# Optimization experiments

Hardware: AMD Instinct MI355X
Metric: run time of the kernel (lower is better)

Reference implementation:

```python
import jax, jax.numpy as jnp
import numpy as np

T, B, D_POSE, H, K_CODES = 30, 1024, 135, 512, 512
EPS = 1e-5


def _bn_relu(x, g, b):
    # BatchNorm1d (training-mode batch stats, biased var) + ReLU; x: (B, C, L)
    m = x.mean(axis=(0, 2), keepdims=True)
    v = x.var(axis=(0, 2), keepdims=True)
    y = g[None, :, None] * (x - m) * jax.lax.rsqrt(v + EPS) + b[None, :, None]
    return jax.nn.relu(y)


def _conv_sk(x, w):
    # Conv1d with stride == kernel_size (non-overlapping): pure reshaped GEMM.
    # x: (B, I, L), w: (O, I, K) torch layout -> (B, O, L//K)
    Bn, I, L = x.shape
    O, _, K = w.shape
    xr = x.reshape(Bn, I, L // K, K)
    return jnp.einsum('bitk,oik->bot', xr, w)


def _convT_sk(x, w):
    # ConvTranspose1d with stride == kernel_size: x (B, I, L), w (I, O, K) torch layout
    Bn, I, L = x.shape
    _, O, K = w.shape
    return jnp.einsum('bil,iok->bolk', x, w).reshape(Bn, O, L * K)


def setup_inputs() -> dict:
    key = jax.random.key(0)
    ks = jax.random.split(key, 12)
    sc = 0.05
    inp = {
        'input_seqs': jax.random.normal(ks[0], (T, B, D_POSE), jnp.float32),
        'W_in': jax.random.normal(ks[1], (D_POSE, H), jnp.float32) * sc,
        'b_in': jnp.zeros((H,), jnp.float32),
        'w_e1': jax.random.normal(ks[2], (H, H, 5), jnp.float32) * sc,
        'g_e1': jnp.ones((H,), jnp.float32), 'b_e1': jnp.zeros((H,), jnp.float32),
        'w_e2': jax.random.normal(ks[3], (H, H, 3), jnp.float32) * sc,
        'g_e2': jnp.ones((H,), jnp.float32), 'b_e2': jnp.zeros((H,), jnp.float32),
        'w_e3': jax.random.normal(ks[4], (H, H, 2), jnp.float32) * sc,
        'g_e3': jnp.ones((H,), jnp.float32), 'b_e3': jnp.zeros((H,), jnp.float32),
        'codebook': jax.random.normal(ks[5], (K_CODES, H), jnp.float32) * sc,
        'W_q': jax.random.normal(ks[6], (H, H), jnp.float32) * sc,
        'b_q': jnp.zeros((H,), jnp.float32),
        'w_d1': jax.random.normal(ks[7], (H, H, 2), jnp.float32) * sc,
        'g_d1': jnp.ones((H,), jnp.float32), 'b_d1': jnp.zeros((H,), jnp.float32),
        'w_d2': jax.random.normal(ks[8], (H, H, 3), jnp.float32) * sc,
        'g_d2': jnp.ones((H,), jnp.float32), 'b_d2': jnp.zeros((H,), jnp.float32),
        'w_d3': jax.random.normal(ks[9], (H, H, 5), jnp.float32) * sc,
        'g_d3': jnp.ones((H,), jnp.float32), 'b_d3': jnp.zeros((H,), jnp.float32),
        'W_out': jax.random.normal(ks[10], (H, D_POSE), jnp.float32) * sc,
        'b_out': jnp.zeros((D_POSE,), jnp.float32),
    }
    return inp


def reference(input_seqs, W_in, b_in, w_e1, g_e1, b_e1, w_e2, g_e2, b_e2,
              w_e3, g_e3, b_e3, codebook, W_q, b_q,
              w_d1, g_d1, b_d1, w_d2, g_d2, b_d2, w_d3, g_d3, b_d3,
              W_out, b_out):
    commitment_cost = 0.25
    # ---- EncoderCNN ----
    h = input_seqs @ W_in + b_in              # (T, B, H)
    h = jnp.transpose(h, (1, 2, 0))           # (B, H, T)
    h = _bn_relu(_conv_sk(h, w_e1), g_e1, b_e1)   # (B, H, 6)
    h = _bn_relu(_conv_sk(h, w_e2), g_e2, b_e2)   # (B, H, 2)
    z = _bn_relu(_conv_sk(h, w_e3), g_e3, b_e3)   # (B, H, 1)

    # ---- VQ (VQ_Payam, straight-through) ----
    Bn, D, L = z.shape
    flat = jnp.transpose(z, (0, 2, 1)).reshape(-1, D)            # (B*L, D)
    dist = (jnp.sum(flat ** 2, axis=1, keepdims=True)
            + jnp.sum(codebook ** 2, axis=1)
            - 2.0 * flat @ codebook.T)                           # (B*L, K)
    idx = jnp.argmin(dist, axis=1)                               # (B*L,)
    quantized = codebook[idx]                                    # (B*L, D)
    e_latent_loss = jnp.mean((jax.lax.stop_gradient(quantized) - flat) ** 2)
    q_latent_loss = jnp.mean((quantized - jax.lax.stop_gradient(flat)) ** 2)
    vq_loss = q_latent_loss + commitment_cost * e_latent_loss
    q_st = flat + jax.lax.stop_gradient(quantized - flat)        # straight-through
    avg_probs = jnp.mean(jax.nn.one_hot(idx, K_CODES, dtype=flat.dtype), axis=0)
    perplexity = jnp.exp(-jnp.sum(avg_probs * jnp.log(avg_probs + 1e-10)))

    # ---- DecoderCNN ----
    d = q_st @ W_q + b_q                      # (B, H)
    d = d[:, :, None]                         # (B, H, 1)
    d = _bn_relu(_convT_sk(d, w_d1), g_d1, b_d1)  # (B, H, 2)
    d = _bn_relu(_convT_sk(d, w_d2), g_d2, b_d2)  # (B, H, 6)
    d = _bn_relu(_convT_sk(d, w_d3), g_d3, b_d3)  # (B, H, 30)
    recon = jnp.transpose(d, (0, 2, 1)) @ W_out + b_out           # (B, T, D_POSE)
    return recon, vq_loss, perplexity
```

## Files before the change

### kernel.cpp

```cpp
#include <hip/hip_runtime.h>
#include <math.h>


#define TM 64
#define TN 64
#define BK 32
#define LSTR 68

typedef __attribute__((ext_vector_type(8))) short bf16x8;
typedef __attribute__((ext_vector_type(4))) float f32x4;

__device__ __forceinline__ unsigned pk_bf16(float a, float b) {
    unsigned ua = __float_as_uint(a), ub = __float_as_uint(b);
    ua += 0x7fffu + ((ua >> 16) & 1u);
    ub += 0x7fffu + ((ub >> 16) & 1u);
    return (ua >> 16) | (ub & 0xffff0000u);
}
__device__ __forceinline__ unsigned short bfh(float x) {
    unsigned u = __float_as_uint(x);
    u += 0x7fffu + ((u >> 16) & 1u);
    return (unsigned short)(u >> 16);
}
__device__ __forceinline__ float bf2f(unsigned short h) {
    return __uint_as_float(((unsigned)h) << 16);
}

template <int NV>
__device__ __forceinline__ void bn_on_raw(uint4* raw, int kbase,
                                          const float* __restrict__ bnS,
                                          const float* __restrict__ bnB) {
#pragma unroll
    for (int i = 0; i < NV; ++i) {
        unsigned* u4 = (unsigned*)&raw[i];
#pragma unroll
        for (int j = 0; j < 4; ++j) {
            const int k = kbase + (i << 3) + (j << 1);
            unsigned u = u4[j];
            float x0 = __uint_as_float(u << 16);
            float x1 = __uint_as_float(u & 0xffff0000u);
            x0 = fmaxf(fmaf(x0, bnS[k],     bnB[k]),     0.f);
            x1 = fmaxf(fmaf(x1, bnS[k + 1], bnB[k + 1]), 0.f);
            u4[j] = pk_bf16(x0, x1);
        }
    }
}

__global__ __launch_bounds__(256)
void k_gemm(const float* __restrict__ Abase,
            const float* __restrict__ Wt,
            float* __restrict__ Cout,
            const float* __restrict__ bias,
            const float* __restrict__ bnS, const float* __restrict__ bnB,
            float* __restrict__ stats,
            unsigned long long* __restrict__ amin,
            const float* __restrict__ codesq,
            int Mslice, int K, int N,
            int n_terms, int enc_mode, int decK)
{
    __shared__ __align__(16) float As[BK][LSTR];
    __shared__ __align__(16) float Bs[BK][LSTR];
    __shared__ float colsum[TN];
    __shared__ float colsq[TN];

    const int tid = threadIdx.x;
    const int z  = blockIdx.z;
    const int n0 = blockIdx.x * TN;
    const int m0 = blockIdx.y * TM;
    const int ty = tid >> 4;
    const int tx = tid & 15;

    if (stats != nullptr && tid < TN) { colsum[tid] = 0.f; colsq[tid] = 0.f; }

    float acc[4][4];
#pragma unroll
    for (int i = 0; i < 4; ++i)
#pragma unroll
        for (int j = 0; j < 4; ++j) acc[i][j] = 0.f;

    const int arow = tid >> 2;
    const int ac4  = (tid & 3) << 2;
    const int brow = tid >> 3;
    const int bc4  = (tid & 7) << 2;

    int mrow = m0 + arow;
    if (mrow > Mslice - 1) mrow = Mslice - 1;

    const bool alignedK = ((K & 31) == 0);

    for (int term = 0; term < n_terms; ++term) {
        int a_slice, wk;
        if (enc_mode) { a_slice = z * n_terms + term; wk = term; }
        else          { a_slice = z / decK;           wk = z % decK; }
        const float* Ap = Abase + (size_t)a_slice * (size_t)Mslice * (size_t)K;
        const float* Wp = Wt    + (size_t)wk * (size_t)K * (size_t)N;
        const float* Arow_p = Ap + (size_t)mrow * (size_t)K;

        for (int k0 = 0; k0 < K; k0 += BK) {
            __syncthreads();
            if (alignedK) {
                float4 a0 = *(const float4*)(Arow_p + k0 + ac4);
                float4 a1 = *(const float4*)(Arow_p + k0 + ac4 + 16);
                if (bnS != nullptr) {
                    float4 s0 = *(const float4*)(bnS + k0 + ac4);
                    float4 c0 = *(const float4*)(bnB + k0 + ac4);
                    float4 s1 = *(const float4*)(bnS + k0 + ac4 + 16);
                    float4 c1 = *(const float4*)(bnB + k0 + ac4 + 16);
                    a0.x = fmaxf(fmaf(a0.x, s0.x, c0.x), 0.f);
                    a0.y = fmaxf(fmaf(a0.y, s0.y, c0.y), 0.f);
                    a0.z = fmaxf(fmaf(a0.z, s0.z, c0.z), 0.f);
                    a0.w = fmaxf(fmaf(a0.w, s0.w, c0.w), 0.f);
                    a1.x = fmaxf(fmaf(a1.x, s1.x, c1.x), 0.f);
                    a1.y = fmaxf(fmaf(a1.y, s1.y, c1.y), 0.f);
                    a1.z = fmaxf(fmaf(a1.z, s1.z, c1.z), 0.f);
                    a1.w = fmaxf(fmaf(a1.w, s1.w, c1.w), 0.f);
                }
                As[ac4+0][arow] = a0.x;  As[ac4+1][arow] = a0.y;
                As[ac4+2][arow] = a0.z;  As[ac4+3][arow] = a0.w;
                As[ac4+16][arow] = a1.x; As[ac4+17][arow] = a1.y;
                As[ac4+18][arow] = a1.z; As[ac4+19][arow] = a1.w;
            } else {
#pragma unroll
                for (int j = 0; j < 4; ++j) {
                    int k = k0 + ac4 + j;
                    As[ac4+j][arow] = (k < K) ? Arow_p[k] : 0.f;
                    int k2 = k + 16;
                    As[ac4+16+j][arow] = (k2 < K) ? Arow_p[k2] : 0.f;
                }
            }
            {
                int kB = k0 + brow;
                float4 b0 = make_float4(0.f, 0.f, 0.f, 0.f);
                float4 b1 = make_float4(0.f, 0.f, 0.f, 0.f);
                if (kB < K) {
                    const float* wrow = Wp + (size_t)kB * N + n0;
                    b0 = *(const float4*)(wrow + bc4);
                    b1 = *(const float4*)(wrow + bc4 + 32);
                }
                *(float4*)&Bs[brow][bc4]      = b0;
                *(float4*)&Bs[brow][bc4 + 32] = b1;
            }
            __syncthreads();
#pragma unroll
            for (int kk = 0; kk < BK; ++kk) {
                float4 av = *(const float4*)&As[kk][ty << 2];
                float4 bv = *(const float4*)&Bs[kk][tx << 2];
                acc[0][0] = fmaf(av.x, bv.x, acc[0][0]);
                acc[0][1] = fmaf(av.x, bv.y, acc[0][1]);
                acc[0][2] = fmaf(av.x, bv.z, acc[0][2]);
                acc[0][3] = fmaf(av.x, bv.w, acc[0][3]);
                acc[1][0] = fmaf(av.y, bv.x, acc[1][0]);
                acc[1][1] = fmaf(av.y, bv.y, acc[1][1]);
                acc[1][2] = fmaf(av.y, bv.z, acc[1][2]);
                acc[1][3] = fmaf(av.y, bv.w, acc[1][3]);
                acc[2][0] = fmaf(av.z, bv.x, acc[2][0]);
                acc[2][1] = fmaf(av.z, bv.y, acc[2][1]);
                acc[2][2] = fmaf(av.z, bv.z, acc[2][2]);
                acc[2][3] = fmaf(av.z, bv.w, acc[2][3]);
                acc[3][0] = fmaf(av.w, bv.x, acc[3][0]);
                acc[3][1] = fmaf(av.w, bv.y, acc[3][1]);
                acc[3][2] = fmaf(av.w, bv.z, acc[3][2]);
                acc[3][3] = fmaf(av.w, bv.w, acc[3][3]);
            }
        }
    }

    if (amin != nullptr) {
        float4 cq = *(const float4*)(codesq + n0 + (tx << 2));
#pragma unroll
        for (int i = 0; i < 4; ++i) {
            int m = m0 + (ty << 2) + i;
            if (m >= Mslice) continue;
            float d0 = cq.x - 2.f * acc[i][0];
            float d1 = cq.y - 2.f * acc[i][1];
            float d2 = cq.z - 2.f * acc[i][2];
            float d3 = cq.w - 2.f * acc[i][3];
            float best = d0; int bj = 0;
            if (d1 < best) { best = d1; bj = 1; }
            if (d2 < best) { best = d2; bj = 2; }
            if (d3 < best) { best = d3; bj = 3; }
            unsigned u = __float_as_uint(best);
            u = (u & 0x80000000u) ? ~u : (u | 0x80000000u);
            unsigned long long key =
                ((unsigned long long)u << 32) | (unsigned)(n0 + (tx << 2) + bj);
            atomicMin(&amin[m], key);
        }
        return;
    }

#pragma unroll
    for (int i = 0; i < 4; ++i) {
        int m = m0 + (ty << 2) + i;
        if (m >= Mslice) continue;
        float4 v = make_float4(acc[i][0], acc[i][1], acc[i][2], acc[i][3]);
        if (bias != nullptr) {
            float4 bb = *(const float4*)(bias + n0 + (tx << 2));
            v.x += bb.x; v.y += bb.y; v.z += bb.z; v.w += bb.w;
        }
        *(float4*)&Cout[((size_t)z * Mslice + m) * N + n0 + (tx << 2)] = v;
    }

    if (stats != nullptr) {
#pragma unroll
        for (int j = 0; j < 4; ++j) {
            float s = 0.f, q = 0.f;
#pragma unroll
            for (int i = 0; i < 4; ++i) {
                int m = m0 + (ty << 2) + i;
                if (m < Mslice) { float x = acc[i][j]; s += x; q += x * x; }
            }
            atomicAdd(&colsum[(tx << 2) + j], s);
            atomicAdd(&colsq [(tx << 2) + j], q);
        }
        __syncthreads();
        if (tid < TN) {
            atomicAdd(&stats[n0 + tid],       colsum[tid]);
            atomicAdd(&stats[512 + n0 + tid], colsq[tid]);
        }
    }
}

#define ASTR 72

__global__ __launch_bounds__(256)
void k_mfma_b(const unsigned short* __restrict__ Abase,
              const unsigned short* __restrict__ Bt,
              unsigned short* __restrict__ Cb,
              float* __restrict__ operm,
              const float* __restrict__ bias,
              const float* __restrict__ bnS, const float* __restrict__ bnB,
              float* __restrict__ stats,
              int Mslice, int K, int N, int decK)
{
    __shared__ __align__(16) unsigned short As[128 * ASTR];
    __shared__ __align__(16) unsigned short Bs[128 * ASTR];
    __shared__ float colsum[128], colsq[128];

    const int tid  = threadIdx.x;
    const int lane = tid & 63;
    const int wave = tid >> 6;
    const int wm = (wave >> 1) << 6;
    const int wn = (wave & 1) << 6;
    const int z  = blockIdx.z;
    const int n0 = blockIdx.x << 7;
    const int m0 = blockIdx.y << 7;

    if (stats != nullptr && tid < 128) { colsum[tid] = 0.f; colsq[tid] = 0.f; }

    const int a_slice = z / decK, wk = z - a_slice * decK;
    const unsigned short* Ap = Abase + (size_t)a_slice * (size_t)Mslice * (size_t)K;
    const unsigned short* Bp = Bt + (size_t)wk * (size_t)N * (size_t)K;

    const int sr = tid >> 1;
    const int sk = (tid & 1) << 5;

    const unsigned short* Arow = Ap + (size_t)(m0 + sr) * K + sk;
    const unsigned short* Brow = Bp + (size_t)(n0 + sr) * K + sk;
    const bool bvalid = (n0 + sr) < N;

    f32x4 acc[4][4];
#pragma unroll
    for (int i = 0; i < 4; ++i)
#pragma unroll
        for (int j = 0; j < 4; ++j) acc[i][j] = (f32x4){0.f, 0.f, 0.f, 0.f};

    const int lidx = lane & 15;
    const int lq   = lane >> 4;

    uint4 pa[4], pb[4];
#pragma unroll
    for (int i = 0; i < 4; ++i) pa[i] = *(const uint4*)(Arow + (i << 3));
    if (bnS != nullptr) bn_on_raw<4>(pa, sk, bnS, bnB);
    if (bvalid) {
#pragma unroll
        for (int i = 0; i < 4; ++i) pb[i] = *(const uint4*)(Brow + (i << 3));
    } else {
#pragma unroll
        for (int i = 0; i < 4; ++i) pb[i] = make_uint4(0u, 0u, 0u, 0u);
    }

    for (int k0 = 0; k0 < K; k0 += 64) {
        __syncthreads();
        {
            uint4* dA = (uint4*)&As[sr * ASTR + sk];
            uint4* dB = (uint4*)&Bs[sr * ASTR + sk];
#pragma unroll
            for (int i = 0; i < 4; ++i) { dA[i] = pa[i]; dB[i] = pb[i]; }
        }
        const int k0n = k0 + 64;
        if (k0n < K) {
#pragma unroll
            for (int i = 0; i < 4; ++i) pa[i] = *(const uint4*)(Arow + k0n + (i << 3));
            if (bnS != nullptr) bn_on_raw<4>(pa, k0n + sk, bnS, bnB);
            if (bvalid) {
#pragma unroll
                for (int i = 0; i < 4; ++i) pb[i] = *(const uint4*)(Brow + k0n + (i << 3));
            }
        }
        __syncthreads();
#pragma unroll
        for (int ks = 0; ks < 2; ++ks) {
            const int kb = (ks << 5) + (lq << 3);
            bf16x8 af[4], bfv[4];
#pragma unroll
            for (int t = 0; t < 4; ++t)
                af[t] = *(const bf16x8*)&As[(wm + (t << 4) + lidx) * ASTR + kb];
#pragma unroll
            for (int t = 0; t < 4; ++t)
                bfv[t] = *(const bf16x8*)&Bs[(wn + (t << 4) + lidx) * ASTR + kb];
#pragma unroll
            for (int mt = 0; mt < 4; ++mt)
#pragma unroll
                for (int nt = 0; nt < 4; ++nt)
                    acc[mt][nt] = __builtin_amdgcn_mfma_f32_16x16x32_bf16(
                        af[mt], bfv[nt], acc[mt][nt], 0, 0, 0);
        }
    }

    const int rbase = lq << 2;
#pragma unroll
    for (int nt = 0; nt < 4; ++nt) {
        const int col = n0 + wn + (nt << 4) + lidx;
        const float badd = (bias != nullptr && col < N) ? bias[col] : 0.f;
        float s = 0.f, q = 0.f;
#pragma unroll
        for (int mt = 0; mt < 4; ++mt) {
#pragma unroll
            for (int r = 0; r < 4; ++r) {
                float x = acc[mt][nt][r];
                s += x; q += x * x;
                const int row = m0 + wm + (mt << 4) + rbase + r;
                if (operm != nullptr) {
                    if (col < N) {
                        const int t = row >> 10, b = row & 1023;
                        operm[(size_t)b * 4050 + t * 135 + col] = x + badd;
                    }
                } else {
                    Cb[((size_t)z * Mslice + row) * (size_t)N + col] = bfh(x + badd);
                }
            }
        }
        if (stats != nullptr) {
            s += __shfl_xor(s, 16, 64); s += __shfl_xor(s, 32, 64);
            q += __shfl_xor(q, 16, 64); q += __shfl_xor(q, 32, 64);
            if (lq == 0) {
                atomicAdd(&colsum[wn + (nt << 4) + lidx], s);
                atomicAdd(&colsq [wn + (nt << 4) + lidx], q);
            }
        }
    }
    if (stats != nullptr) {
        __syncthreads();
        if (tid < 128) {
            atomicAdd(&stats[n0 + tid],       colsum[tid]);
            atomicAdd(&stats[512 + n0 + tid], colsq[tid]);
        }
    }
}

#define BSTR 72

__global__ __launch_bounds__(256)
void k_b64(const unsigned short* __restrict__ Abase,
           const unsigned short* __restrict__ Bt,
           unsigned short* __restrict__ Cb,
           const float* __restrict__ bias,
           const float* __restrict__ bnS, const float* __restrict__ bnB,
           float* __restrict__ stats,
           int Mslice, int K, int N, int decK)
{
    __shared__ __align__(16) unsigned short As[64 * BSTR];
    __shared__ __align__(16) unsigned short Bs[64 * BSTR];
    __shared__ float colsum[64], colsq[64];

    const int tid  = threadIdx.x;
    const int lane = tid & 63;
    const int wave = tid >> 6;
    const int wm = (wave >> 1) << 5;
    const int wn = (wave & 1) << 5;
    const int z  = blockIdx.z;
    const int n0 = blockIdx.x << 6;
    const int m0 = blockIdx.y << 6;

    if (stats != nullptr && tid < 64) { colsum[tid] = 0.f; colsq[tid] = 0.f; }

    const int a_slice = z / decK, wk = z - a_slice * decK;
    const unsigned short* Ap = Abase + (size_t)a_slice * (size_t)Mslice * (size_t)K;
    const unsigned short* Bp = Bt + (size_t)wk * (size_t)N * (size_t)K;

    const int sr = tid >> 2;
    const int sk = (tid & 3) << 4;

    const unsigned short* Arow = Ap + (size_t)(m0 + sr) * K + sk;
    const unsigned short* Brow = Bp + (size_t)(n0 + sr) * K + sk;

    f32x4 acc[2][2];
#pragma unroll
    for (int i = 0; i < 2; ++i)
#pragma unroll
        for (int j = 0; j < 2; ++j) acc[i][j] = (f32x4){0.f, 0.f, 0.f, 0.f};

    const int lidx = lane & 15;
    const int lq   = lane >> 4;

    uint4 pa[2], pb[2];
    pa[0] = *(const uint4*)(Arow);
    pa[1] = *(const uint4*)(Arow + 8);
    if (bnS != nullptr) bn_on_raw<2>(pa, sk, bnS, bnB);
    pb[0] = *(const uint4*)(Brow);
    pb[1] = *(const uint4*)(Brow + 8);

    for (int k0 = 0; k0 < K; k0 += 64) {
        __syncthreads();
        {
            uint4* dA = (uint4*)&As[sr * BSTR + sk];
            uint4* dB = (uint4*)&Bs[sr * BSTR + sk];
            dA[0] = pa[0]; dA[1] = pa[1];
            dB[0] = pb[0]; dB[1] = pb[1];
        }
        const int k0n = k0 + 64;
        if (k0n < K) {
            pa[0] = *(const uint4*)(Arow + k0n);
            pa[1] = *(const uint4*)(Arow + k0n + 8);
            if (bnS != nullptr) bn_on_raw<2>(pa, k0n + sk, bnS, bnB);
            pb[0] = *(const uint4*)(Brow + k0n);
            pb[1] = *(const uint4*)(Brow + k0n + 8);
        }
        __syncthreads();
#pragma unroll
        for (int ks = 0; ks < 2; ++ks) {
            const int kb = (ks << 5) + (lq << 3);
            bf16x8 af[2], bfv[2];
#pragma unroll
            for (int t = 0; t < 2; ++t)
                af[t] = *(const bf16x8*)&As[(wm + (t << 4) + lidx) * BSTR + kb];
#pragma unroll
            for (int t = 0; t < 2; ++t)
                bfv[t] = *(const bf16x8*)&Bs[(wn + (t << 4) + lidx) * BSTR + kb];
#pragma unroll
            for (int mt = 0; mt < 2; ++mt)
#pragma unroll
                for (int nt = 0; nt < 2; ++nt)
                    acc[mt][nt] = __builtin_amdgcn_mfma_f32_16x16x32_bf16(
                        af[mt], bfv[nt], acc[mt][nt], 0, 0, 0);
        }
    }

    const int rbase = lq << 2;
#pragma unroll
    for (int nt = 0; nt < 2; ++nt) {
        const int col = n0 + wn + (nt << 4) + lidx;
        const float badd = (bias != nullptr) ? bias[col] : 0.f;
        float s = 0.f, q = 0.f;
#pragma unroll
        for (int mt = 0; mt < 2; ++mt) {
#pragma unroll
            for (int r = 0; r < 4; ++r) {
                float x = acc[mt][nt][r];
                s += x; q += x * x;
                const int row = m0 + wm + (mt << 4) + rbase + r;
                Cb[((size_t)z * Mslice + row) * (size_t)N + col] = bfh(x + badd);
            }
        }
        if (stats != nullptr) {
            s += __shfl_xor(s, 16, 64); s += __shfl_xor(s, 32, 64);
            q += __shfl_xor(q, 16, 64); q += __shfl_xor(q, 32, 64);
            if (lq == 0) {
                atomicAdd(&colsum[wn + (nt << 4) + lidx], s);
                atomicAdd(&colsq [wn + (nt << 4) + lidx], q);
            }
        }
    }
    if (stats != nullptr) {
        __syncthreads();
        if (tid < 64) {
            atomicAdd(&stats[n0 + tid],       colsum[tid]);
            atomicAdd(&stats[512 + n0 + tid], colsq[tid]);
        }
    }
}

#define S64 40

__global__ __launch_bounds__(256)
void k_sp64(const unsigned short* __restrict__ Ahg,
            const unsigned short* __restrict__ Alg,
            const unsigned short* __restrict__ Whi,
            const unsigned short* __restrict__ Wlo,
            float* __restrict__ Cout, float* __restrict__ stats,
            int Mslice, int Kp, int N, int n_terms)
{
    __shared__ __align__(16) unsigned short Ah[64 * S64];
    __shared__ __align__(16) unsigned short Al[64 * S64];
    __shared__ __align__(16) unsigned short Bh[64 * S64];
    __shared__ __align__(16) unsigned short Bl[64 * S64];
    __shared__ float colsum[64], colsq[64];

    const int tid  = threadIdx.x;
    const int lane = tid & 63;
    const int wave = tid >> 6;
    const int wm = (wave >> 1) << 5;
    const int wn = (wave & 1) << 5;
    const int z  = blockIdx.z;
    const int n0 = blockIdx.x << 6;
    const int m0 = blockIdx.y << 6;

    if (stats != nullptr && tid < 64) { colsum[tid] = 0.f; colsq[tid] = 0.f; }

    const int sr = tid >> 2;
    const int sk = (tid & 3) << 3;

    f32x4 acc[2][2];
#pragma unroll
    for (int i = 0; i < 2; ++i)
#pragma unroll
        for (int j = 0; j < 2; ++j) acc[i][j] = (f32x4){0.f, 0.f, 0.f, 0.f};

    const int lidx = lane & 15;
    const int lq   = lane >> 4;
    const int kb   = lq << 3;

    const int cpk = Kp >> 5;
    const int tot = n_terms * cpk;

    uint4 rah, ral, rbh, rblv;
    {
        const size_t ab = ((size_t)(z * n_terms) * Mslice + m0 + sr) * (size_t)Kp + sk;
        rah = *(const uint4*)(Ahg + ab);
        ral = *(const uint4*)(Alg + ab);
        const size_t bb = ((size_t)(n0 + sr)) * (size_t)Kp + sk;
        rbh = *(const uint4*)(Whi + bb);
        rblv = *(const uint4*)(Wlo + bb);
    }
    int lt = 0, lk = 32;
    if (lk >= Kp) { lk = 0; lt = 1; }

    for (int c = 0; c < tot; ++c) {
        __syncthreads();
        *(uint4*)&Ah[sr * S64 + sk] = rah;
        *(uint4*)&Al[sr * S64 + sk] = ral;
        *(uint4*)&Bh[sr * S64 + sk] = rbh;
        *(uint4*)&Bl[sr * S64 + sk] = rblv;
        if (c + 1 < tot) {
            const size_t ab = ((size_t)(z * n_terms + lt) * Mslice + m0 + sr) * (size_t)Kp + lk + sk;
            rah = *(const uint4*)(Ahg + ab);
            ral = *(const uint4*)(Alg + ab);
            const size_t bb = ((size_t)lt * N + n0 + sr) * (size_t)Kp + lk + sk;
            rbh = *(const uint4*)(Whi + bb);
            rblv = *(const uint4*)(Wlo + bb);
            lk += 32; if (lk >= Kp) { lk = 0; ++lt; }
        }
        __syncthreads();
        bf16x8 ah[2], al[2], bh[2], bl[2];
#pragma unroll
        for (int t = 0; t < 2; ++t) {
            const int ra = (wm + (t << 4) + lidx) * S64 + kb;
            ah[t] = *(const bf16x8*)&Ah[ra];
            al[t] = *(const bf16x8*)&Al[ra];
        }
#pragma unroll
        for (int t = 0; t < 2; ++t) {
            const int rb = (wn + (t << 4) + lidx) * S64 + kb;
            bh[t] = *(const bf16x8*)&Bh[rb];
            bl[t] = *(const bf16x8*)&Bl[rb];
        }
#pragma unroll
        for (int mt = 0; mt < 2; ++mt)
#pragma unroll
            for (int nt = 0; nt < 2; ++nt) {
                acc[mt][nt] = __builtin_amdgcn_mfma_f32_16x16x32_bf16(
                    ah[mt], bh[nt], acc[mt][nt], 0, 0, 0);
                acc[mt][nt] = __builtin_amdgcn_mfma_f32_16x16x32_bf16(
                    al[mt], bh[nt], acc[mt][nt], 0, 0, 0);
                acc[mt][nt] = __builtin_amdgcn_mfma_f32_16x16x32_bf16(
                    ah[mt], bl[nt], acc[mt][nt], 0, 0, 0);
            }
    }

    const int rbase = lq << 2;
#pragma unroll
    for (int nt = 0; nt < 2; ++nt) {
        const int col = n0 + wn + (nt << 4) + lidx;
        float s = 0.f, q = 0.f;
#pragma unroll
        for (int mt = 0; mt < 2; ++mt) {
#pragma unroll
            for (int r = 0; r < 4; ++r) {
                float x = acc[mt][nt][r];
                s += x; q += x * x;
                const int row = m0 + wm + (mt << 4) + rbase + r;
                Cout[((size_t)z * Mslice + row) * (size_t)N + col] = x;
            }
        }
        if (stats != nullptr) {
            s += __shfl_xor(s, 16, 64); s += __shfl_xor(s, 32, 64);
            q += __shfl_xor(q, 16, 64); q += __shfl_xor(q, 32, 64);
            if (lq == 0) {
                atomicAdd(&colsum[wn + (nt << 4) + lidx], s);
                atomicAdd(&colsq [wn + (nt << 4) + lidx], q);
            }
        }
    }
    if (stats != nullptr) {
        __syncthreads();
        if (tid < 64) {
            atomicAdd(&stats[n0 + tid],       colsum[tid]);
            atomicAdd(&stats[512 + n0 + tid], colsq[tid]);
        }
    }
}

__global__ void k_prep(float* __restrict__ zbase, unsigned long long* __restrict__ amin,
                       const float* __restrict__ codebook, float* __restrict__ codeT,
                       float* __restrict__ codesq,
                       const float* __restrict__ w_e2, unsigned short* __restrict__ whi_e2,
                       unsigned short* __restrict__ wlo_e2,
                       const float* __restrict__ w_e3, unsigned short* __restrict__ whi_e3,
                       unsigned short* __restrict__ wlo_e3,
                       const float* __restrict__ W_q,  unsigned short* __restrict__ wqb,
                       const float* __restrict__ w_d1, unsigned short* __restrict__ wd1b,
                       const float* __restrict__ w_d2, unsigned short* __restrict__ wd2b,
                       const float* __restrict__ w_d3, unsigned short* __restrict__ wd3b,
                       const float* __restrict__ W_out, unsigned short* __restrict__ woutb,
                       const float* __restrict__ in_seqs,
                       unsigned short* __restrict__ in_h, unsigned short* __restrict__ in_l)
{
    __shared__ float red[4];
    const int bid = blockIdx.x;
    const int tid = threadIdx.x;

    if (bid < 32) {
        int t = bid * 256 + tid;
        if (t < 6720) zbase[t] = 0.f;
        if (t < 1024) amin[t] = ~0ULL;
        return;
    }
    if (bid < 1056) {
        int idx = (bid - 32) * 256 + tid;
        int i = (idx >> 9) & 511, o = idx & 511;
        codeT[idx] = codebook[(o << 9) + i];
        return;
    }
    if (bid < 1568) {
        int c = bid - 1056;
        float s = 0.f;
        for (int i = tid; i < 512; i += 256) { float v = codebook[c * 512 + i]; s += v * v; }
        for (int off = 32; off; off >>= 1) s += __shfl_down(s, off, 64);
        if ((tid & 63) == 0) red[tid >> 6] = s;
        __syncthreads();
        if (tid == 0) codesq[c] = red[0] + red[1] + red[2] + red[3];
        return;
    }
    if (bid < 4640) {
        int idx = (bid - 1568) * 256 + tid;
        int i = idx & 511, o = (idx >> 9) & 511, k = idx >> 18;
        float v = w_e2[(((o << 9) + i) * 3) + k];
        unsigned short h = bfh(v);
        whi_e2[idx] = h; wlo_e2[idx] = bfh(v - bf2f(h));
        return;
    }
    if (bid < 6688) {
        int idx = (bid - 4640) * 256 + tid;
        int i = idx & 511, o = (idx >> 9) & 511, k = idx >> 18;
        float v = w_e3[(((o << 9) + i) * 2) + k];
        unsigned short h = bfh(v);
        whi_e3[idx] = h; wlo_e3[idx] = bfh(v - bf2f(h));
        return;
    }
    if (bid < 7712) {
        int idx = (bid - 6688) * 256 + tid;
        int i = idx & 511, o = (idx >> 9) & 511;
        wqb[idx] = bfh(W_q[((size_t)i << 9) + o]);
        return;
    }
    if (bid < 9760) {
        int idx = (bid - 7712) * 256 + tid;
        int i = idx & 511, o = (idx >> 9) & 511, k = idx >> 18;
        wd1b[idx] = bfh(w_d1[(((size_t)i << 9) + o) * 2 + k]);
        return;
    }
    if (bid < 12832) {
        int idx = (bid - 9760) * 256 + tid;
        int i = idx & 511, o = (idx >> 9) & 511, k = idx >> 18;
        wd2b[idx] = bfh(w_d2[(((size_t)i << 9) + o) * 3 + k]);
        return;
    }
    if (bid < 17952) {
        int idx = (bid - 12832) * 256 + tid;
        int i = idx & 511, o = (idx >> 9) & 511, k = idx >> 18;
        wd3b[idx] = bfh(w_d3[(((size_t)i << 9) + o) * 5 + k]);
        return;
    }
    if (bid < 18222) {
        int idx = (bid - 17952) * 256 + tid;
        if (idx >= 69120) return;
        int i = idx % 512, o = idx / 512;
        woutb[idx] = bfh(W_out[((size_t)i * 135) + o]);
        return;
    }
    {
        int idx = (bid - 18222) * 256 + tid;
        if (idx >= 4915200) return;
        int i = idx % 160, r = idx / 160;
        float v = (i < 135) ? in_seqs[(size_t)r * 135 + i] : 0.f;
        unsigned short h = bfh(v);
        in_h[idx] = h; in_l[idx] = bfh(v - bf2f(h));
    }
}

__global__ void k_repack(const float* __restrict__ w, float* __restrict__ wt,
                         int Kc, int total)
{
    int idx = blockIdx.x * 256 + threadIdx.x;
    if (idx >= total) return;
    int k = idx >> 18;
    int rem = idx & 262143;
    int i = rem >> 9, o = rem & 511;
    wt[idx] = w[(((o << 9) + i) * Kc + k)];
}

__global__ void k_repack_sp_weff(const float* __restrict__ weff,
                                 unsigned short* __restrict__ whi,
                                 unsigned short* __restrict__ wlo,
                                 int total)
{
    int idx = blockIdx.x * 256 + threadIdx.x;
    if (idx >= total) return;
    int i = idx % 160;
    int o = (idx / 160) & 511;
    int t = idx / 81920;
    float v = (i < 135) ? weff[((size_t)t * 135 + i) * 512 + o] : 0.f;
    unsigned short h = bfh(v);
    whi[idx] = h;
    wlo[idx] = bfh(v - bf2f(h));
}

__global__ void k_bnsplit(const float* __restrict__ x,
                          const float* __restrict__ sc, const float* __restrict__ sh,
                          unsigned short* __restrict__ hq, unsigned short* __restrict__ lq_,
                          int total4)
{
    int idx = blockIdx.x * 256 + threadIdx.x;
    if (idx >= total4) return;
    const int base = idx << 2;
    float4 f = *(const float4*)(x + base);
    const int k = base & 511;
    float4 s = *(const float4*)(sc + k);
    float4 c = *(const float4*)(sh + k);
    float y0 = fmaxf(fmaf(f.x, s.x, c.x), 0.f);
    float y1 = fmaxf(fmaf(f.y, s.y, c.y), 0.f);
    float y2 = fmaxf(fmaf(f.z, s.z, c.z), 0.f);
    float y3 = fmaxf(fmaf(f.w, s.w, c.w), 0.f);
    unsigned short h0 = bfh(y0), h1 = bfh(y1), h2 = bfh(y2), h3 = bfh(y3);
    unsigned short l0 = bfh(y0 - bf2f(h0)), l1 = bfh(y1 - bf2f(h1));
    unsigned short l2 = bfh(y2 - bf2f(h2)), l3 = bfh(y3 - bf2f(h3));
    *(uint2*)&hq[base]  = make_uint2((unsigned)h0 | ((unsigned)h1 << 16),
                                     (unsigned)h2 | ((unsigned)h3 << 16));
    *(uint2*)&lq_[base] = make_uint2((unsigned)l0 | ((unsigned)l1 << 16),
                                     (unsigned)l2 | ((unsigned)l3 << 16));
}

__global__ void k_bnapply(const unsigned short* __restrict__ x,
                          const float* __restrict__ sc, const float* __restrict__ sh,
                          unsigned short* __restrict__ y, int total8)
{
    int idx = blockIdx.x * 256 + threadIdx.x;
    if (idx >= total8) return;
    const int base = idx << 3;
    uint4 raw = *(const uint4*)(x + base);
    const int k = base & 511;
    float4 s0 = *(const float4*)(sc + k);
    float4 c0 = *(const float4*)(sh + k);
    float4 s1 = *(const float4*)(sc + k + 4);
    float4 c1 = *(const float4*)(sh + k + 4);
    unsigned* u = (unsigned*)&raw;
    float x0 = __uint_as_float(u[0] << 16),        x1 = __uint_as_float(u[0] & 0xffff0000u);
    float x2 = __uint_as_float(u[1] << 16),        x3 = __uint_as_float(u[1] & 0xffff0000u);
    float x4 = __uint_as_float(u[2] << 16),        x5 = __uint_as_float(u[2] & 0xffff0000u);
    float x6 = __uint_as_float(u[3] << 16),        x7 = __uint_as_float(u[3] & 0xffff0000u);
    x0 = fmaxf(fmaf(x0, s0.x, c0.x), 0.f); x1 = fmaxf(fmaf(x1, s0.y, c0.y), 0.f);
    x2 = fmaxf(fmaf(x2, s0.z, c0.z), 0.f); x3 = fmaxf(fmaf(x3, s0.w, c0.w), 0.f);
    x4 = fmaxf(fmaf(x4, s1.x, c1.x), 0.f); x5 = fmaxf(fmaf(x5, s1.y, c1.y), 0.f);
    x6 = fmaxf(fmaf(x6, s1.z, c1.z), 0.f); x7 = fmaxf(fmaf(x7, s1.w, c1.w), 0.f);
    *(uint4*)&y[base] = make_uint4(pk_bf16(x0, x1), pk_bf16(x2, x3),
                                   pk_bf16(x4, x5), pk_bf16(x6, x7));
}

__global__ void k_bn_fin(const float* __restrict__ stats,
                         const float* __restrict__ g, const float* __restrict__ b,
                         float* __restrict__ sc, float* __restrict__ sh, float inv_n)
{
    int c = blockIdx.x * blockDim.x + threadIdx.x;
    if (c >= 512) return;
    float m = stats[c] * inv_n;
    float v = stats[512 + c] * inv_n - m * m;
    float a = (float)((double)g[c] / sqrt((double)v + 1e-5));
    sc[c] = a;
    sh[c] = b[c] - m * a;
}

__global__ void k_vq_gather(const unsigned long long* __restrict__ amin,
                            const float* __restrict__ codebook,
                            const float* __restrict__ e3pre,
                            const float* __restrict__ sc, const float* __restrict__ sh,
                            unsigned short* __restrict__ quant_bf,
                            float* __restrict__ loss,
                            unsigned int* __restrict__ hist)
{
    int b = blockIdx.x; int t = threadIdx.x;
    unsigned int idx = (unsigned int)(amin[b] & 0xFFFFFFFFull) & 511u;
    float part = 0.f;
    for (int i = t; i < 512; i += 256) {
        float q = codebook[(size_t)idx * 512 + i];
        quant_bf[(size_t)b * 512 + i] = bfh(q);
        float x = e3pre[(size_t)b * 512 + i];
        float f = fmaxf(fmaf(x, sc[i], sh[i]), 0.f);
        float d = q - f;
        part += d * d;
    }
    for (int off = 32; off; off >>= 1) part += __shfl_down(part, off, 64);
    __shared__ float red[4];
    if ((t & 63) == 0) red[t >> 6] = part;
    __syncthreads();
    if (t == 0) {
        atomicAdd(loss, red[0] + red[1] + red[2] + red[3]);
        atomicAdd(&hist[idx], 1u);
    }
}

__global__ void k_scalars(const unsigned int* __restrict__ hist,
                          const float* __restrict__ loss, float* __restrict__ out)
{
    int t = threadIdx.x;
    float p = (float)hist[t] * (1.0f / 1024.0f);
    float e = p * logf(p + 1e-10f);
    for (int off = 32; off; off >>= 1) e += __shfl_down(e, off, 64);
    __shared__ float red[8];
    if ((t & 63) == 0) red[t >> 6] = e;
    __syncthreads();
    if (t == 0) {
        float s = 0.f;
        for (int i = 0; i < 8; ++i) s += red[i];
        out[4147200] = 1.25f * loss[0] * (1.0f / 524288.0f);
        out[4147201] = expf(-s);
    }
}

extern "C" void kernel_launch(void* const* d_in, const int* in_sizes, int n_in,
                              void* d_out, int out_size, void* d_ws, size_t ws_size,
                              hipStream_t stream)
{
    const float* in_seqs = (const float*)d_in[0];
    const float* W_in  = (const float*)d_in[1];
    const float* w_e1  = (const float*)d_in[3];
    const float* g_e1  = (const float*)d_in[4];
    const float* be1   = (const float*)d_in[5];
    const float* w_e2  = (const float*)d_in[6];
    const float* g_e2  = (const float*)d_in[7];
    const float* be2   = (const float*)d_in[8];
    const float* w_e3  = (const float*)d_in[9];
    const float* g_e3  = (const float*)d_in[10];
    const float* be3   = (const float*)d_in[11];
    const float* codebook = (const float*)d_in[12];
    const float* W_q   = (const float*)d_in[13];
    const float* b_q   = (const float*)d_in[14];
    const float* w_d1  = (const float*)d_in[15];
    const float* g_d1  = (const float*)d_in[16];
    const float* bd1   = (const float*)d_in[17];
    const float* w_d2  = (const float*)d_in[18];
    const float* g_d2  = (const float*)d_in[19];
    const float* bd2   = (const float*)d_in[20];
    const float* w_d3  = (const float*)d_in[21];
    const float* g_d3  = (const float*)d_in[22];
    const float* bd3   = (const float*)d_in[23];
    const float* W_out = (const float*)d_in[24];
    const float* b_out = (const float*)d_in[25];
    float* out = (float*)d_out;

    float* W = (float*)d_ws;
    unsigned long long* amin = (unsigned long long*)W;
    float* stats  = W + 2048;
    float* lossp  = W + 8192;
    unsigned int* hist = (unsigned int*)(W + 8256);
    float* scsh   = W + 8768;
    float* codesq = W + 14912;
    float* wt_e1  = W + 15424;
    float* weff   = W + 1326144;
    float* codeT  = W + 1671744;
    unsigned short* esw = (unsigned short*)(W + 1933888);
    unsigned short* whi_e1 = esw;
    unsigned short* wlo_e1 = esw + 409600;
    unsigned short* whi_e2 = esw + 819200;
    unsigned short* wlo_e2 = esw + 1605632;
    unsigned short* whi_e3 = esw + 2392064;
    unsigned short* wlo_e3 = esw + 2916352;
    unsigned short* in_h  = (unsigned short*)(W + 3654208);
    unsigned short* in_l  = in_h + 4915200;
    unsigned short* d3pre = (unsigned short*)(W + 3654208);
    float* e1f = W + 11518528;
    unsigned short* e1h = (unsigned short*)(W + 14664256);
    unsigned short* e1l = e1h + 3145728;
    float* e2f = W + 17809984;
    unsigned short* e2h = (unsigned short*)(W + 18858560);
    unsigned short* e2l = e2h + 1048576;
    unsigned short* d2pre = (unsigned short*)(W + 17809984);
    unsigned short* d2bf  = d2pre + 3145728;
    float* e3f = W + 20955712;
    unsigned short* quant_bf = (unsigned short*)(W + 21480000);
    unsigned short* d0bf     = (unsigned short*)(W + 21742144);
    unsigned short* d1pre    = (unsigned short*)(W + 22004288);

    unsigned short* db    = (unsigned short*)wt_e1;
    unsigned short* wqb   = db;
    unsigned short* wd1b  = db + 262144;
    unsigned short* wd2b  = db + 786432;
    unsigned short* wd3b  = db + 1572864;
    unsigned short* woutb = db + 2883584;

    float* st_e1 = stats + 0 * 1024; float* sc_e1 = scsh + 0 * 1024; float* sh_e1 = sc_e1 + 512;
    float* st_e2 = stats + 1 * 1024; float* sc_e2 = scsh + 1 * 1024; float* sh_e2 = sc_e2 + 512;
    float* st_e3 = stats + 2 * 1024; float* sc_e3 = scsh + 2 * 1024; float* sh_e3 = sc_e3 + 512;
    float* st_d1 = stats + 3 * 1024; float* sc_d1 = scsh + 3 * 1024; float* sh_d1 = sc_d1 + 512;
    float* st_d2 = stats + 4 * 1024; float* sc_d2 = scsh + 4 * 1024; float* sh_d2 = sc_d2 + 512;
    float* st_d3 = stats + 5 * 1024; float* sc_d3 = scsh + 5 * 1024; float* sh_d3 = sc_d3 + 512;

    dim3 blk(256);

    k_repack<<<dim3(5 * 1024), blk, 0, stream>>>(w_e1, wt_e1, 5, 5 * 262144);
    k_gemm<<<dim3(8, 3, 5), blk, 0, stream>>>(W_in, wt_e1, weff, nullptr,
        nullptr, nullptr, nullptr, nullptr, nullptr, 135, 512, 512, 1, 0, 5);
    k_repack_sp_weff<<<dim3(1600), blk, 0, stream>>>(weff, whi_e1, wlo_e1, 409600);

    k_prep<<<dim3(37422), blk, 0, stream>>>(stats, amin,
        codebook, codeT, codesq,
        w_e2, whi_e2, wlo_e2, w_e3, whi_e3, wlo_e3,
        W_q, wqb, w_d1, wd1b, w_d2, wd2b, w_d3, wd3b, W_out, woutb,
        in_seqs, in_h, in_l);

    k_sp64<<<dim3(8, 16, 6), blk, 0, stream>>>(in_h, in_l, whi_e1, wlo_e1,
        e1f, st_e1, 1024, 160, 512, 5);
    k_bn_fin<<<dim3(2), blk, 0, stream>>>(st_e1, g_e1, be1, sc_e1, sh_e1, 1.f / 6144.f);
    k_bnsplit<<<dim3(3072), blk, 0, stream>>>(e1f, sc_e1, sh_e1, e1h, e1l, 786432);

    k_sp64<<<dim3(8, 16, 2), blk, 0, stream>>>(e1h, e1l, whi_e2, wlo_e2,
        e2f, st_e2, 1024, 512, 512, 3);
    k_bn_fin<<<dim3(2), blk, 0, stream>>>(st_e2, g_e2, be2, sc_e2, sh_e2, 1.f / 2048.f);
    k_bnsplit<<<dim3(1024), blk, 0, stream>>>(e2f, sc_e2, sh_e2, e2h, e2l, 262144);

    k_sp64<<<dim3(8, 16, 1), blk, 0, stream>>>(e2h, e2l, whi_e3, wlo_e3,
        e3f, st_e3, 1024, 512, 512, 2);
    k_bn_fin<<<dim3(2), blk, 0, stream>>>(st_e3, g_e3, be3, sc_e3, sh_e3, 1.f / 1024.f);

    k_gemm<<<dim3(8, 16, 1), blk, 0, stream>>>(e3f, codeT, nullptr, nullptr,
        sc_e3, sh_e3, nullptr, amin, codesq, 1024, 512, 512, 1, 1, 1);
    k_vq_gather<<<dim3(1024), blk, 0, stream>>>(amin, codebook, e3f, sc_e3, sh_e3,
                                                quant_bf, lossp, hist);

    k_b64<<<dim3(8, 16, 1), blk, 0, stream>>>(quant_bf, wqb, d0bf,
        b_q, nullptr, nullptr, nullptr, 1024, 512, 512, 1);

    k_b64<<<dim3(8, 16, 2), blk, 0, stream>>>(d0bf, wd1b, d1pre,
        nullptr, nullptr, nullptr, st_d1, 1024, 512, 512, 2);
    k_bn_fin<<<dim3(2), blk, 0, stream>>>(st_d1, g_d1, bd1, sc_d1, sh_d1, 1.f / 2048.f);

    k_b64<<<dim3(8, 16, 6), blk, 0, stream>>>(d1pre, wd2b, d2pre,
        nullptr, sc_d1, sh_d1, st_d2, 1024, 512, 512, 3);
    k_bn_fin<<<dim3(2), blk, 0, stream>>>(st_d2, g_d2, bd2, sc_d2, sh_d2, 1.f / 6144.f);

    k_bnapply<<<dim3(1536), blk, 0, stream>>>(d2pre, sc_d2, sh_d2, d2bf, 393216);

    k_mfma_b<<<dim3(4, 8, 30), blk, 0, stream>>>(d2bf, wd3b, d3pre, nullptr,
        nullptr, nullptr, nullptr, st_d3, 1024, 512, 512, 5);
    k_bn_fin<<<dim3(2), blk, 0, stream>>>(st_d3, g_d3, bd3, sc_d3, sh_d3, 1.f / 30720.f);

    k_mfma_b<<<dim3(2, 240, 1), blk, 0, stream>>>(d3pre, woutb, nullptr, out,
        b_out, sc_d3, sh_d3, nullptr, 30720, 512, 135, 1);

    k_scalars<<<dim3(1), dim3(512), 0, stream>>>(hist, lossp, out);
}
```

Measured before the change: 493.1 us.

## Shrink fp32 GEMM tiles to 32x32 with register prefetch and wave-reduced argmin

The fp32 k_gemm is reworked from 64x64 tiles with a 4x4 micro-tile to 32x32 tiles with a 2x2 micro-tile, which quadruples the block count for the small W_in*w_e1 product and the codebook distance GEMM. The next K-slice of A and B is prefetched into registers while the current slice is computed. The VQ argmin now reduces keys across 16 lanes with shuffles before a single atomicMin per row, cutting global atomic traffic. Unused bias/stats/enc_mode paths are removed. The cost is lower per-thread arithmetic intensity and more shared-memory traffic per FMA.

```diff
diff --git a/kernel.cpp b/kernel.cpp
--- a/kernel.cpp
+++ b/kernel.cpp
@@ -1,11 +1,6 @@
 #include <hip/hip_runtime.h>
 #include <math.h>
 
-
-#define TM 64
-#define TN 64
-#define BK 32
-#define LSTR 68
 
 typedef __attribute__((ext_vector_type(8))) short bf16x8;
 typedef __attribute__((ext_vector_type(4))) float f32x4;
@@ -45,176 +40,110 @@
     }
 }
 
+__device__ __forceinline__ void bn4(float4& a, const float* __restrict__ s,
+                                    const float* __restrict__ c) {
+    float4 sv = *(const float4*)s;
+    float4 cv = *(const float4*)c;
+    a.x = fmaxf(fmaf(a.x, sv.x, cv.x), 0.f);
+    a.y = fmaxf(fmaf(a.y, sv.y, cv.y), 0.f);
+    a.z = fmaxf(fmaf(a.z, sv.z, cv.z), 0.f);
+    a.w = fmaxf(fmaf(a.w, sv.w, cv.w), 0.f);
+}
+
+#define FBK  32
+#define FSTR 36
+
 __global__ __launch_bounds__(256)
 void k_gemm(const float* __restrict__ Abase,
             const float* __restrict__ Wt,
             float* __restrict__ Cout,
-            const float* __restrict__ bias,
             const float* __restrict__ bnS, const float* __restrict__ bnB,
-            float* __restrict__ stats,
             unsigned long long* __restrict__ amin,
             const float* __restrict__ codesq,
-            int Mslice, int K, int N,
-            int n_terms, int enc_mode, int decK)
-{
-    __shared__ __align__(16) float As[BK][LSTR];
-    __shared__ __align__(16) float Bs[BK][LSTR];
-    __shared__ float colsum[TN];
-    __shared__ float colsq[TN];
+            int Mslice, int K, int N, int decK)
+{
+    __shared__ __align__(16) float As[FBK][FSTR];
+    __shared__ __align__(16) float Bs[FBK][FSTR];
 
     const int tid = threadIdx.x;
     const int z  = blockIdx.z;
-    const int n0 = blockIdx.x * TN;
-    const int m0 = blockIdx.y * TM;
+    const int n0 = blockIdx.x << 5;
+    const int m0 = blockIdx.y << 5;
     const int ty = tid >> 4;
     const int tx = tid & 15;
 
-    if (stats != nullptr && tid < TN) { colsum[tid] = 0.f; colsq[tid] = 0.f; }
-
-    float acc[4][4];
-#pragma unroll
-    for (int i = 0; i < 4; ++i)
-#pragma unroll
-        for (int j = 0; j < 4; ++j) acc[i][j] = 0.f;
-
-    const int arow = tid >> 2;
-    const int ac4  = (tid & 3) << 2;
-    const int brow = tid >> 3;
-    const int bc4  = (tid & 7) << 2;
-
-    int mrow = m0 + arow;
+    const int a_slice = z / decK, wk = z - a_slice * decK;
+    const float* Ap = Abase + (size_t)a_slice * (size_t)Mslice * (size_t)K;
+    const float* Wp = Wt    + (size_t)wk * (size_t)K * (size_t)N;
+
+    const int sr  = tid >> 3;
+    const int sc4 = (tid & 7) << 2;
+
+    int mrow = m0 + sr;
     if (mrow > Mslice - 1) mrow = Mslice - 1;
-
-    const bool alignedK = ((K & 31) == 0);
-
-    for (int term = 0; term < n_terms; ++term) {
-        int a_slice, wk;
-        if (enc_mode) { a_slice = z * n_terms + term; wk = term; }
-        else          { a_slice = z / decK;           wk = z % decK; }
-        const float* Ap = Abase + (size_t)a_slice * (size_t)Mslice * (size_t)K;
-        const float* Wp = Wt    + (size_t)wk * (size_t)K * (size_t)N;
-        const float* Arow_p = Ap + (size_t)mrow * (size_t)K;
-
-        for (int k0 = 0; k0 < K; k0 += BK) {
-            __syncthreads();
-            if (alignedK) {
-                float4 a0 = *(const float4*)(Arow_p + k0 + ac4);
-                float4 a1 = *(const float4*)(Arow_p + k0 + ac4 + 16);
-                if (bnS != nullptr) {
-                    float4 s0 = *(const float4*)(bnS + k0 + ac4);
-                    float4 c0 = *(const float4*)(bnB + k0 + ac4);
-                    float4 s1 = *(const float4*)(bnS + k0 + ac4 + 16);
-                    float4 c1 = *(const float4*)(bnB + k0 + ac4 + 16);
-                    a0.x = fmaxf(fmaf(a0.x, s0.x, c0.x), 0.f);
-                    a0.y = fmaxf(fmaf(a0.y, s0.y, c0.y), 0.f);
-                    a0.z = fmaxf(fmaf(a0.z, s0.z, c0.z), 0.f);
-                    a0.w = fmaxf(fmaf(a0.w, s0.w, c0.w), 0.f);
-                    a1.x = fmaxf(fmaf(a1.x, s1.x, c1.x), 0.f);
-                    a1.y = fmaxf(fmaf(a1.y, s1.y, c1.y), 0.f);
-                    a1.z = fmaxf(fmaf(a1.z, s1.z, c1.z), 0.f);
-                    a1.w = fmaxf(fmaf(a1.w, s1.w, c1.w), 0.f);
-                }
-                As[ac4+0][arow] = a0.x;  As[ac4+1][arow] = a0.y;
-                As[ac4+2][arow] = a0.z;  As[ac4+3][arow] = a0.w;
-                As[ac4+16][arow] = a1.x; As[ac4+17][arow] = a1.y;
-                As[ac4+18][arow] = a1.z; As[ac4+19][arow] = a1.w;
-            } else {
-#pragma unroll
-                for (int j = 0; j < 4; ++j) {
-                    int k = k0 + ac4 + j;
-                    As[ac4+j][arow] = (k < K) ? Arow_p[k] : 0.f;
-                    int k2 = k + 16;
-                    As[ac4+16+j][arow] = (k2 < K) ? Arow_p[k2] : 0.f;
-                }
-            }
-            {
-                int kB = k0 + brow;
-                float4 b0 = make_float4(0.f, 0.f, 0.f, 0.f);
-                float4 b1 = make_float4(0.f, 0.f, 0.f, 0.f);
-                if (kB < K) {
-                    const float* wrow = Wp + (size_t)kB * N + n0;
-                    b0 = *(const float4*)(wrow + bc4);
-                    b1 = *(const float4*)(wrow + bc4 + 32);
-                }
-                *(float4*)&Bs[brow][bc4]      = b0;
-                *(float4*)&Bs[brow][bc4 + 32] = b1;
-            }
-            __syncthreads();
-#pragma unroll
-            for (int kk = 0; kk < BK; ++kk) {
-                float4 av = *(const float4*)&As[kk][ty << 2];
-                float4 bv = *(const float4*)&Bs[kk][tx << 2];
-                acc[0][0] = fmaf(av.x, bv.x, acc[0][0]);
-                acc[0][1] = fmaf(av.x, bv.y, acc[0][1]);
-                acc[0][2] = fmaf(av.x, bv.z, acc[0][2]);
-                acc[0][3] = fmaf(av.x, bv.w, acc[0][3]);
-                acc[1][0] = fmaf(av.y, bv.x, acc[1][0]);
-                acc[1][1] = fmaf(av.y, bv.y, acc[1][1]);
-                acc[1][2] = fmaf(av.y, bv.z, acc[1][2]);
-                acc[1][3] = fmaf(av.y, bv.w, acc[1][3]);
-                acc[2][0] = fmaf(av.z, bv.x, acc[2][0]);
-                acc[2][1] = fmaf(av.z, bv.y, acc[2][1]);
-                acc[2][2] = fmaf(av.z, bv.z, acc[2][2]);
-                acc[2][3] = fmaf(av.z, bv.w, acc[2][3]);
-                acc[3][0] = fmaf(av.w, bv.x, acc[3][0]);
-                acc[3][1] = fmaf(av.w, bv.y, acc[3][1]);
-                acc[3][2] = fmaf(av.w, bv.z, acc[3][2]);
-                acc[3][3] = fmaf(av.w, bv.w, acc[3][3]);
-            }
+    const float* Arow_p = Ap + (size_t)mrow * K;
+
+    float acc[2][2];
+    acc[0][0] = 0.f; acc[0][1] = 0.f; acc[1][0] = 0.f; acc[1][1] = 0.f;
+
+    float4 pa = *(const float4*)(Arow_p + sc4);
+    if (bnS != nullptr) bn4(pa, bnS + sc4, bnB + sc4);
+    float4 pb = *(const float4*)(Wp + (size_t)sr * N + n0 + sc4);
+
+    for (int k0 = 0; k0 < K; k0 += FBK) {
+        __syncthreads();
+        As[sc4 + 0][sr] = pa.x;
+        As[sc4 + 1][sr] = pa.y;
+        As[sc4 + 2][sr] = pa.z;
+        As[sc4 + 3][sr] = pa.w;
+        *(float4*)&Bs[sr][sc4] = pb;
+        const int k0n = k0 + FBK;
+        if (k0n < K) {
+            pa = *(const float4*)(Arow_p + k0n + sc4);
+            if (bnS != nullptr) bn4(pa, bnS + k0n + sc4, bnB + k0n + sc4);
+            pb = *(const float4*)(Wp + (size_t)(k0n + sr) * N + n0 + sc4);
+        }
+        __syncthreads();
+#pragma unroll
+        for (int kk = 0; kk < FBK; ++kk) {
+            float2 av = *(const float2*)&As[kk][ty << 1];
+            float2 bv = *(const float2*)&Bs[kk][tx << 1];
+            acc[0][0] = fmaf(av.x, bv.x, acc[0][0]);
+            acc[0][1] = fmaf(av.x, bv.y, acc[0][1]);
+            acc[1][0] = fmaf(av.y, bv.x, acc[1][0]);
+            acc[1][1] = fmaf(av.y, bv.y, acc[1][1]);
         }
     }
 
     if (amin != nullptr) {
-        float4 cq = *(const float4*)(codesq + n0 + (tx << 2));
-#pragma unroll
-        for (int i = 0; i < 4; ++i) {
-            int m = m0 + (ty << 2) + i;
-            if (m >= Mslice) continue;
+        float2 cq = *(const float2*)(codesq + n0 + (tx << 1));
+#pragma unroll
+        for (int i = 0; i < 2; ++i) {
+            const int m = m0 + (ty << 1) + i;
             float d0 = cq.x - 2.f * acc[i][0];
             float d1 = cq.y - 2.f * acc[i][1];
-            float d2 = cq.z - 2.f * acc[i][2];
-            float d3 = cq.w - 2.f * acc[i][3];
-            float best = d0; int bj = 0;
-            if (d1 < best) { best = d1; bj = 1; }
-            if (d2 < best) { best = d2; bj = 2; }
-            if (d3 < best) { best = d3; bj = 3; }
+            int bj = (d1 < d0) ? 1 : 0;
+            float best = (d1 < d0) ? d1 : d0;
             unsigned u = __float_as_uint(best);
             u = (u & 0x80000000u) ? ~u : (u | 0x80000000u);
             unsigned long long key =
-                ((unsigned long long)u << 32) | (unsigned)(n0 + (tx << 2) + bj);
-            atomicMin(&amin[m], key);
-        }
-        return;
-    }
-
-#pragma unroll
-    for (int i = 0; i < 4; ++i) {
-        int m = m0 + (ty << 2) + i;
-        if (m >= Mslice) continue;
-        float4 v = make_float4(acc[i][0], acc[i][1], acc[i][2], acc[i][3]);
-        if (bias != nullptr) {
-            float4 bb = *(const float4*)(bias + n0 + (tx << 2));
-            v.x += bb.x; v.y += bb.y; v.z += bb.z; v.w += bb.w;
-        }
-        *(float4*)&Cout[((size_t)z * Mslice + m) * N + n0 + (tx << 2)] = v;
-    }
-
-    if (stats != nullptr) {
-#pragma unroll
-        for (int j = 0; j < 4; ++j) {
-            float s = 0.f, q = 0.f;
-#pragma unroll
-            for (int i = 0; i < 4; ++i) {
-                int m = m0 + (ty << 2) + i;
-                if (m < Mslice) { float x = acc[i][j]; s += x; q += x * x; }
+                ((unsigned long long)u << 32) | (unsigned)(n0 + (tx << 1) + bj);
+#pragma unroll
+            for (int off = 1; off < 16; off <<= 1) {
+                unsigned long long o = __shfl_xor(key, off, 64);
+                if (o < key) key = o;
             }
-            atomicAdd(&colsum[(tx << 2) + j], s);
-            atomicAdd(&colsq [(tx << 2) + j], q);
-        }
-        __syncthreads();
-        if (tid < TN) {
-            atomicAdd(&stats[n0 + tid],       colsum[tid]);
-            atomicAdd(&stats[512 + n0 + tid], colsq[tid]);
+            if (tx == 0 && m < Mslice) atomicMin(&amin[m], key);
+        }
+        return;
+    }
+
+#pragma unroll
+    for (int i = 0; i < 2; ++i) {
+        const int m = m0 + (ty << 1) + i;
+        if (m < Mslice) {
+            float2 v = make_float2(acc[i][0], acc[i][1]);
+            *(float2*)&Cout[((size_t)z * Mslice + m) * N + n0 + (tx << 1)] = v;
         }
     }
 }
@@ -926,8 +855,8 @@
     dim3 blk(256);
 
     k_repack<<<dim3(5 * 1024), blk, 0, stream>>>(w_e1, wt_e1, 5, 5 * 262144);
-    k_gemm<<<dim3(8, 3, 5), blk, 0, stream>>>(W_in, wt_e1, weff, nullptr,
-        nullptr, nullptr, nullptr, nullptr, nullptr, 135, 512, 512, 1, 0, 5);
+    k_gemm<<<dim3(16, 5, 5), blk, 0, stream>>>(W_in, wt_e1, weff,
+        nullptr, nullptr, nullptr, nullptr, 135, 512, 512, 5);
     k_repack_sp_weff<<<dim3(1600), blk, 0, stream>>>(weff, whi_e1, wlo_e1, 409600);
 
     k_prep<<<dim3(37422), blk, 0, stream>>>(stats, amin,
@@ -950,8 +879,8 @@
         e3f, st_e3, 1024, 512, 512, 2);
     k_bn_fin<<<dim3(2), blk, 0, stream>>>(st_e3, g_e3, be3, sc_e3, sh_e3, 1.f / 1024.f);
 
-    k_gemm<<<dim3(8, 16, 1), blk, 0, stream>>>(e3f, codeT, nullptr, nullptr,
-        sc_e3, sh_e3, nullptr, amin, codesq, 1024, 512, 512, 1, 1, 1);
+    k_gemm<<<dim3(16, 32, 1), blk, 0, stream>>>(e3f, codeT, nullptr,
+        sc_e3, sh_e3, amin, codesq, 1024, 512, 512, 1);
     k_vq_gather<<<dim3(1024), blk, 0, stream>>>(amin, codebook, e3f, sc_e3, sh_e3,
                                                 quant_bf, lossp, hist);
 
```

Measured after the change: 457.3 us. 7.3% less time.
